# Kernel tuning notes

Measured on AMD Instinct MI355X. Metric: run time of the kernel, lower is better.

The kernel has to match this reference:

```python
import jax, jax.numpy as jnp
import numpy as np

N_NODES = 100000
N_EDGES = 3200000  # avg degree 32
NFEAT = 512
NOUT = 7
DIMS = [NFEAT, 12, 10, 8, 6, 4, NOUT]  # hard-coded hidden widths from __init__


def setup_inputs() -> dict:
    key = jax.random.key(0)
    ks = jax.random.split(key, 4 + 2 * 6)
    inp = {
        "x": jax.random.normal(ks[0], (N_NODES, NFEAT), dtype=jnp.float32),
        "edge_val": jax.random.uniform(ks[1], (N_EDGES,), dtype=jnp.float32) / 32.0,  # ~normalized adj
        "edge_src": jax.random.randint(ks[2], (N_EDGES,), 0, N_NODES),
        "edge_dst": jax.random.randint(ks[3], (N_EDGES,), 0, N_NODES),
    }
    for i in range(6):
        s = 1.0 / np.sqrt(DIMS[i + 1])  # pygcn reset_parameters: U(-1/sqrt(out), 1/sqrt(out))
        inp[f"W{i+1}"] = jax.random.uniform(ks[4 + 2 * i], (DIMS[i], DIMS[i + 1]), jnp.float32, -s, s)
        inp[f"b{i+1}"] = jax.random.uniform(ks[5 + 2 * i], (DIMS[i + 1],), jnp.float32, -s, s)
    return inp


def reference(x, edge_val, W1, b1, W2, b2, W3, b3, W4, b4, W5, b5, W6, b6,
              edge_src, edge_dst):
    n = x.shape[0]

    def gc(h, W, b):
        s = h @ W                                   # [N, out] dense mm
        m = edge_val[:, None] * s[edge_src]         # gather + scale per edge
        agg = jax.ops.segment_sum(m, edge_dst, num_segments=n)  # spmm scatter
        return agg + b

    tanhshrink = lambda v: v - jnp.tanh(v)

    h = gc(x, W1, b1)                # dropout p=0 -> identity
    h = jax.nn.relu(gc(h, W2, b2))   # eval-mode dropout -> identity
    h = tanhshrink(gc(h, W3, b3))
    h = tanhshrink(gc(h, W4, b4))
    h = gc(h, W5, b5)
    return gc(h, W6, b6)
```

## Files before the change

### kernel.cpp

```cpp
#include <hip/hip_runtime.h>
#include <math.h>
#include <stdint.h>


#define T_EDGES 12800
#define NB_MAX  1600
#define FCAP    2560
#define OTSTR   72
#define KIT     10
#define MAXIT   336

__global__ __launch_bounds__(512) void hist_kernel(const int* __restrict__ dst,
                                                   int* __restrict__ ghist, int E, int NB) {
    __shared__ int h[NB_MAX];
    for (int i = threadIdx.x; i < NB; i += 512) h[i] = 0;
    __syncthreads();
    int base = blockIdx.x * T_EDGES;
    int n = min(T_EDGES, E - base);
    for (int i = threadIdx.x; i < n; i += 512)
        atomicAdd(&h[((unsigned)dst[base + i]) >> 6], 1);
    __syncthreads();
    for (int i = threadIdx.x; i < NB; i += 512)
        ghist[(size_t)blockIdx.x * NB + i] = h[i];
}

__global__ __launch_bounds__(256) void scanC_kernel(const int* __restrict__ ghist,
                                                    int* __restrict__ goff,
                                                    int* __restrict__ btot, int NT, int NB) {
    __shared__ int part[256];
    int b = blockIdx.x, t = threadIdx.x;
    int v = (t < NT) ? ghist[(size_t)t * NB + b] : 0;
    part[t] = v;
    __syncthreads();
    for (int off = 1; off < 256; off <<= 1) {
        int x = (t >= off) ? part[t - off] : 0;
        __syncthreads();
        part[t] += x;
        __syncthreads();
    }
    if (t < NT) goff[(size_t)t * NB + b] = b * FCAP + part[t] - v;
    if (t == 255) btot[b] = part[255];
}

__global__ __launch_bounds__(1024) void scatter_kernel(const int* __restrict__ src,
                                                       const int* __restrict__ dst,
                                                       const float* __restrict__ val,
                                                       const int* __restrict__ ghist,
                                                       const int* __restrict__ goff,
                                                       int2* __restrict__ edges, int E, int NB) {
    __shared__ unsigned perm[T_EDGES];
    __shared__ int loff[NB_MAX];
    __shared__ int lcur[NB_MAX];
    __shared__ int part[1024];
    int tb = blockIdx.x, t = threadIdx.x;
    int base = tb * T_EDGES;
    int n = min(T_EDGES, E - base);

    int chunk = (NB + 1023) / 1024;
    int lo = t * chunk, hi = min(lo + chunk, NB);
    int s = 0;
    for (int i = lo; i < hi; i++) {
        int c = ghist[(size_t)tb * NB + i];
        loff[i] = c;
        s += c;
    }
    part[t] = s;
    __syncthreads();
    for (int off = 1; off < 1024; off <<= 1) {
        int x = (t >= off) ? part[t - off] : 0;
        __syncthreads();
        part[t] += x;
        __syncthreads();
    }
    int run = part[t] - s;
    for (int i = lo; i < hi; i++) {
        int c = loff[i];
        loff[i] = run;
        lcur[i] = run;
        run += c;
    }
    __syncthreads();

    for (int i = t; i < n; i += 1024) {
        int d = dst[base + i];
        unsigned b = ((unsigned)d) >> 6;
        int p = atomicAdd(&lcur[b], 1);
        perm[p] = (unsigned)i | (b << 14) | ((unsigned)(d & 63) << 25);
    }
    __syncthreads();

    for (int o = t; o < n; o += 1024) {
        unsigned v = perm[o];
        int li = v & 16383;
        int b  = (v >> 14) & 2047;
        int ld = v >> 25;
        int g  = goff[(size_t)tb * NB + b] + (o - loff[b]);
        edges[g] = make_int2(src[base + li] | (ld << 17), __float_as_int(val[base + li]));
    }
}

__global__ __launch_bounds__(512) void finalize_kernel(int2* __restrict__ edges,
                                                       const int* __restrict__ btot,
                                                       int* __restrict__ offsTab) {
    __shared__ int2 recs[FCAP];
    __shared__ int2 recs2[FCAP];
    __shared__ int cnt[64], offs[64], cur[64];
    int b = blockIdx.x, t = threadIdx.x;
    size_t s0 = (size_t)b * FCAP;
    int ne = min(btot[b], FCAP);
    if (t < 64) cnt[t] = 0;
    __syncthreads();
    for (int i = t; i < ne; i += 512) {
        int2 r = edges[s0 + i];
        recs[i] = r;
        atomicAdd(&cnt[(r.x >> 17) & 63], 1);
    }
    __syncthreads();
    if (t == 0) {
        int run = 0;
        for (int i = 0; i < 64; i++) { offs[i] = run; run += cnt[i]; }
    }
    __syncthreads();
    if (t < 64) cur[t] = offs[t];
    __syncthreads();
    for (int i = t; i < ne; i += 512) {
        int2 r = recs[i];
        int ld = (r.x >> 17) & 63;
        int p = atomicAdd(&cur[ld], 1);
        recs2[p] = r;
    }
    __syncthreads();
    for (int i = t; i < ne; i += 512) edges[s0 + i] = recs2[i];
    if (t < 64) offsTab[(size_t)b * OTSTR + t] = offs[t];
    if (t == 64) offsTab[(size_t)b * OTSTR + 64] = ne;
}

__global__ __launch_bounds__(256) void dense1_kernel(const float* __restrict__ x,
                                                     const float* __restrict__ W,
                                                     float* __restrict__ out, int N) {
    __shared__ float xs[256 * 33];
    const int t    = threadIdx.x;
    const int row0 = blockIdx.x * 256;
    const int r    = row0 + t;

    float acc[12];
#pragma unroll
    for (int j = 0; j < 12; j++) acc[j] = 0.f;

    for (int tile = 0; tile < 16; ++tile) {
#pragma unroll
        for (int i = 0; i < 8; i++) {
            int idx4 = t + 256 * i;
            int flat = idx4 * 4;
            int rl   = flat >> 5;
            int c    = flat & 31;
            int rg   = row0 + rl;
            if (rg >= N) rg = N - 1;
            const float4 v = *(const float4*)(x + (size_t)rg * 512 + tile * 32 + c);
            float* p = &xs[rl * 33 + c];
            p[0] = v.x; p[1] = v.y; p[2] = v.z; p[3] = v.w;
        }
        __syncthreads();
#pragma unroll 8
        for (int kk = 0; kk < 32; ++kk) {
            float xv = xs[t * 33 + kk];
            int k = tile * 32 + kk;
#pragma unroll
            for (int j = 0; j < 12; j++) acc[j] += xv * W[k * 12 + j];
        }
        __syncthreads();
    }
    if (r < N) {
        float4* orow = (float4*)(out + (size_t)r * 16);
        orow[0] = make_float4(acc[0], acc[1], acc[2], acc[3]);
        orow[1] = make_float4(acc[4], acc[5], acc[6], acc[7]);
        orow[2] = make_float4(acc[8], acc[9], acc[10], acc[11]);
        orow[3] = make_float4(0.f, 0.f, 0.f, 0.f);
    }
}

template <int SV, int ANV, int DIN, int DOUT, int OSTR, int ACT, bool FINAL>
__global__ __launch_bounds__(256) void layer_kernel(const int2* __restrict__ edges,
                                                    const int* __restrict__ offsTab,
                                                    const float* __restrict__ s,
                                                    const float* __restrict__ bias,
                                                    const float* __restrict__ W,
                                                    float* __restrict__ out, int N) {
    constexpr int ASTR = 13;
    __shared__ int2  ebuf[FCAP];
    __shared__ float acc[64 * ASTR];
    __shared__ int   offs[65];
    __shared__ int   items[MAXIT];
    __shared__ int   nitems_s;
    const int b = blockIdx.x, t = threadIdx.x;
    const int ne = offsTab[(size_t)b * OTSTR + 64];

    for (int i = t; i < 64 * ASTR; i += 256) acc[i] = 0.f;
    for (int i = t; i < ne; i += 256) ebuf[i] = edges[(size_t)b * FCAP + i];
    if (t < 65) offs[t] = offsTab[(size_t)b * OTSTR + t];
    if (t == 0) nitems_s = 0;
    __syncthreads();

    if (t < 64) {
        int st = offs[t];
        int c  = ((t == 63) ? ne : offs[t + 1]) - st;
        if (c > 0) {
            int ni  = (c + KIT - 1) / KIT;
            int pos = atomicAdd(&nitems_s, ni);
            for (int j = 0; j < ni; j++) {
                int len = min(KIT, c - j * KIT);
                items[pos + j] = ((st + j * KIT) << 10) | (len << 6) | t;
            }
        }
    }
    __syncthreads();

    const int nit = nitems_s;
    const float4* sv = (const float4*)s;
    for (int j = t; j < nit; j += 256) {
        int it = items[j];
        int ld    = it & 63;
        int lenm1 = ((it >> 6) & 15) - 1;
        int st    = it >> 10;
        float4 a[ANV];
#pragma unroll
        for (int v = 0; v < ANV; v++) a[v] = make_float4(0.f, 0.f, 0.f, 0.f);
#pragma unroll
        for (int k = 0; k < KIT; k++) {
            int idx = st + min(k, lenm1);
            int2 ev = ebuf[idx];
            float w = (k <= lenm1) ? __int_as_float(ev.y) : 0.f;
            const float4* srow = sv + (size_t)(ev.x & 0x1FFFF) * SV;
#pragma unroll
            for (int v = 0; v < ANV; v++) {
                float4 xr = srow[v];
                a[v].x += w * xr.x; a[v].y += w * xr.y;
                a[v].z += w * xr.z; a[v].w += w * xr.w;
            }
        }
#pragma unroll
        for (int v = 0; v < ANV; v++) {
            atomicAdd(&acc[ld * ASTR + 4 * v + 0], a[v].x);
            atomicAdd(&acc[ld * ASTR + 4 * v + 1], a[v].y);
            atomicAdd(&acc[ld * ASTR + 4 * v + 2], a[v].z);
            atomicAdd(&acc[ld * ASTR + 4 * v + 3], a[v].w);
        }
    }
    __syncthreads();

    if (t < 64) {
        int node = (b << 6) + t;
        if (node < N) {
            float h[DIN];
#pragma unroll
            for (int k = 0; k < DIN; k++) {
                float z = acc[t * ASTR + k] + bias[k];
                if (ACT == 1) z = fmaxf(z, 0.f);
                else if (ACT == 2) z = z - tanhf(z);
                h[k] = z;
            }
            if (FINAL) {
#pragma unroll
                for (int k = 0; k < DIN; k++) out[(size_t)node * DIN + k] = h[k];
            } else {
                float o[OSTR];
#pragma unroll
                for (int j = 0; j < OSTR; j++) o[j] = 0.f;
#pragma unroll
                for (int j = 0; j < DOUT; j++) {
                    float tj = 0.f;
#pragma unroll
                    for (int k = 0; k < DIN; k++) tj += h[k] * W[k * DOUT + j];
                    o[j] = tj;
                }
                float4* orow = (float4*)(out + (size_t)node * OSTR);
#pragma unroll
                for (int v = 0; v < OSTR / 4; v++)
                    orow[v] = make_float4(o[4 * v], o[4 * v + 1], o[4 * v + 2], o[4 * v + 3]);
            }
        }
    }
}


static inline size_t align256(size_t x) { return (x + 255) & ~(size_t)255; }

extern "C" void kernel_launch(void* const* d_in, const int* in_sizes, int n_in,
                              void* d_out, int out_size, void* d_ws, size_t ws_size,
                              hipStream_t stream) {
    const float* x        = (const float*)d_in[0];
    const float* edge_val = (const float*)d_in[1];
    const int*   edge_src = (const int*)d_in[2];
    const int*   edge_dst = (const int*)d_in[3];
    const float* W1 = (const float*)d_in[4];   const float* b1 = (const float*)d_in[5];
    const float* W2 = (const float*)d_in[6];   const float* b2 = (const float*)d_in[7];
    const float* W3 = (const float*)d_in[8];   const float* b3 = (const float*)d_in[9];
    const float* W4 = (const float*)d_in[10];  const float* b4 = (const float*)d_in[11];
    const float* W5 = (const float*)d_in[12];  const float* b5 = (const float*)d_in[13];
    const float* W6 = (const float*)d_in[14];  const float* b6 = (const float*)d_in[15];

    const int N = in_sizes[0] / 512;
    const int E = in_sizes[1];
    float* out = (float*)d_out;

    const int NB = (N + 63) >> 6;
    const int NT = (E + T_EDGES - 1) / T_EDGES;
    const int nb = (N + 255) / 256;

    char* w = (char*)d_ws;
    float* A       = (float*)w;  w += align256((size_t)N * 16 * sizeof(float));
    float* B       = (float*)w;  w += align256((size_t)N * 16 * sizeof(float));
    int*   ghist   = (int*)w;    w += align256((size_t)NT * NB * sizeof(int));
    int*   goff    = (int*)w;    w += align256((size_t)NT * NB * sizeof(int));
    int*   btot    = (int*)w;    w += align256((size_t)NB * sizeof(int));
    int*   offsTab = (int*)w;    w += align256((size_t)NB * OTSTR * sizeof(int));
    int2*  edges   = (int2*)w;   w += align256((size_t)NB * FCAP * sizeof(int2));

    hist_kernel<<<NT, 512, 0, stream>>>(edge_dst, ghist, E, NB);
    scanC_kernel<<<NB, 256, 0, stream>>>(ghist, goff, btot, NT, NB);
    scatter_kernel<<<NT, 1024, 0, stream>>>(edge_src, edge_dst, edge_val, ghist, goff, edges, E, NB);
    finalize_kernel<<<NB, 512, 0, stream>>>(edges, btot, offsTab);

    dense1_kernel<<<nb, 256, 0, stream>>>(x, W1, A, N);

    layer_kernel<4, 3, 12, 10, 16, 0, false><<<NB, 256, 0, stream>>>(edges, offsTab, A, b1, W2, B, N);
    layer_kernel<4, 3, 10, 8, 8, 1, false><<<NB, 256, 0, stream>>>(edges, offsTab, B, b2, W3, A, N);
    layer_kernel<2, 2, 8, 6, 8, 2, false><<<NB, 256, 0, stream>>>(edges, offsTab, A, b3, W4, B, N);
    layer_kernel<2, 2, 6, 4, 4, 2, false><<<NB, 256, 0, stream>>>(edges, offsTab, B, b4, W5, A, N);
    layer_kernel<1, 1, 4, 7, 8, 0, false><<<NB, 256, 0, stream>>>(edges, offsTab, A, b5, W6, B, N);
    layer_kernel<2, 2, 7, 7, 8, 0, true><<<NB, 256, 0, stream>>>(edges, offsTab, B, b6, (const float*)nullptr, out, N);
}
```

Before: 728.2 us.

## Drop per-node edge sort; accumulate each edge directly with LDS atomics

Removes the finalize kernel that sorted each 64-node bucket's edges by local destination and built an offset table. The layer kernels now stream edges straight from global memory two at a time (int4 loads) and do one shared-memory atomicAdd per edge per feature, instead of building per-destination work items and summing up to ten edges in registers before each atomic. This removes a kernel launch, a global read/write pass over the edges, and the staging of edges in LDS. In exchange it issues about ten times more LDS atomics per layer, with possible contention when edges in a wave share a destination.

```diff
diff --git a/kernel.cpp b/kernel.cpp
--- a/kernel.cpp
+++ b/kernel.cpp
@@ -6,9 +6,6 @@
 #define T_EDGES 12800
 #define NB_MAX  1600
 #define FCAP    2560
-#define OTSTR   72
-#define KIT     10
-#define MAXIT   336
 
 __global__ __launch_bounds__(512) void hist_kernel(const int* __restrict__ dst,
                                                    int* __restrict__ ghist, int E, int NB) {
@@ -99,42 +96,6 @@
     }
 }
 
-__global__ __launch_bounds__(512) void finalize_kernel(int2* __restrict__ edges,
-                                                       const int* __restrict__ btot,
-                                                       int* __restrict__ offsTab) {
-    __shared__ int2 recs[FCAP];
-    __shared__ int2 recs2[FCAP];
-    __shared__ int cnt[64], offs[64], cur[64];
-    int b = blockIdx.x, t = threadIdx.x;
-    size_t s0 = (size_t)b * FCAP;
-    int ne = min(btot[b], FCAP);
-    if (t < 64) cnt[t] = 0;
-    __syncthreads();
-    for (int i = t; i < ne; i += 512) {
-        int2 r = edges[s0 + i];
-        recs[i] = r;
-        atomicAdd(&cnt[(r.x >> 17) & 63], 1);
-    }
-    __syncthreads();
-    if (t == 0) {
-        int run = 0;
-        for (int i = 0; i < 64; i++) { offs[i] = run; run += cnt[i]; }
-    }
-    __syncthreads();
-    if (t < 64) cur[t] = offs[t];
-    __syncthreads();
-    for (int i = t; i < ne; i += 512) {
-        int2 r = recs[i];
-        int ld = (r.x >> 17) & 63;
-        int p = atomicAdd(&cur[ld], 1);
-        recs2[p] = r;
-    }
-    __syncthreads();
-    for (int i = t; i < ne; i += 512) edges[s0 + i] = recs2[i];
-    if (t < 64) offsTab[(size_t)b * OTSTR + t] = offs[t];
-    if (t == 64) offsTab[(size_t)b * OTSTR + 64] = ne;
-}
-
 __global__ __launch_bounds__(256) void dense1_kernel(const float* __restrict__ x,
                                                      const float* __restrict__ W,
                                                      float* __restrict__ out, int N) {
@@ -179,71 +140,56 @@
     }
 }
 
-template <int SV, int ANV, int DIN, int DOUT, int OSTR, int ACT, bool FINAL>
+template <int SV, int NACC, int DIN, int DOUT, int OSTR, int ACT, bool FINAL>
 __global__ __launch_bounds__(256) void layer_kernel(const int2* __restrict__ edges,
-                                                    const int* __restrict__ offsTab,
+                                                    const int* __restrict__ btot,
                                                     const float* __restrict__ s,
                                                     const float* __restrict__ bias,
                                                     const float* __restrict__ W,
                                                     float* __restrict__ out, int N) {
     constexpr int ASTR = 13;
-    __shared__ int2  ebuf[FCAP];
     __shared__ float acc[64 * ASTR];
-    __shared__ int   offs[65];
-    __shared__ int   items[MAXIT];
-    __shared__ int   nitems_s;
     const int b = blockIdx.x, t = threadIdx.x;
-    const int ne = offsTab[(size_t)b * OTSTR + 64];
+    const int ne = min(btot[b], FCAP);
 
     for (int i = t; i < 64 * ASTR; i += 256) acc[i] = 0.f;
-    for (int i = t; i < ne; i += 256) ebuf[i] = edges[(size_t)b * FCAP + i];
-    if (t < 65) offs[t] = offsTab[(size_t)b * OTSTR + t];
-    if (t == 0) nitems_s = 0;
-    __syncthreads();
-
-    if (t < 64) {
-        int st = offs[t];
-        int c  = ((t == 63) ? ne : offs[t + 1]) - st;
-        if (c > 0) {
-            int ni  = (c + KIT - 1) / KIT;
-            int pos = atomicAdd(&nitems_s, ni);
-            for (int j = 0; j < ni; j++) {
-                int len = min(KIT, c - j * KIT);
-                items[pos + j] = ((st + j * KIT) << 10) | (len << 6) | t;
-            }
-        }
-    }
-    __syncthreads();
-
-    const int nit = nitems_s;
+    __syncthreads();
+
     const float4* sv = (const float4*)s;
-    for (int j = t; j < nit; j += 256) {
-        int it = items[j];
-        int ld    = it & 63;
-        int lenm1 = ((it >> 6) & 15) - 1;
-        int st    = it >> 10;
-        float4 a[ANV];
-#pragma unroll
-        for (int v = 0; v < ANV; v++) a[v] = make_float4(0.f, 0.f, 0.f, 0.f);
-#pragma unroll
-        for (int k = 0; k < KIT; k++) {
-            int idx = st + min(k, lenm1);
-            int2 ev = ebuf[idx];
-            float w = (k <= lenm1) ? __int_as_float(ev.y) : 0.f;
-            const float4* srow = sv + (size_t)(ev.x & 0x1FFFF) * SV;
-#pragma unroll
-            for (int v = 0; v < ANV; v++) {
+    const int4*   ep = (const int4*)(edges + (size_t)b * FCAP);
+    const int nh = (ne + 1) >> 1;
+#pragma unroll 2
+    for (int i = t; i < nh; i += 256) {
+        int4 e2 = ep[i];
+
+        {
+            int   sidx = e2.x & 0x1FFFF;
+            int   ld   = (e2.x >> 17) & 63;
+            float w    = __int_as_float(e2.y);
+            const float4* srow = sv + (size_t)sidx * SV;
+#pragma unroll
+            for (int v = 0; v < NACC; v++) {
                 float4 xr = srow[v];
-                a[v].x += w * xr.x; a[v].y += w * xr.y;
-                a[v].z += w * xr.z; a[v].w += w * xr.w;
-            }
-        }
-#pragma unroll
-        for (int v = 0; v < ANV; v++) {
-            atomicAdd(&acc[ld * ASTR + 4 * v + 0], a[v].x);
-            atomicAdd(&acc[ld * ASTR + 4 * v + 1], a[v].y);
-            atomicAdd(&acc[ld * ASTR + 4 * v + 2], a[v].z);
-            atomicAdd(&acc[ld * ASTR + 4 * v + 3], a[v].w);
+                atomicAdd(&acc[ld * ASTR + 4 * v + 0], w * xr.x);
+                atomicAdd(&acc[ld * ASTR + 4 * v + 1], w * xr.y);
+                atomicAdd(&acc[ld * ASTR + 4 * v + 2], w * xr.z);
+                atomicAdd(&acc[ld * ASTR + 4 * v + 3], w * xr.w);
+            }
+        }
+        {
+            bool  val  = (2 * i + 1) < ne;
+            int   sidx = val ? (e2.z & 0x1FFFF) : 0;
+            int   ld   = (e2.z >> 17) & 63;
+            float w    = val ? __int_as_float(e2.w) : 0.f;
+            const float4* srow = sv + (size_t)sidx * SV;
+#pragma unroll
+            for (int v = 0; v < NACC; v++) {
+                float4 xr = srow[v];
+                atomicAdd(&acc[ld * ASTR + 4 * v + 0], w * xr.x);
+                atomicAdd(&acc[ld * ASTR + 4 * v + 1], w * xr.y);
+                atomicAdd(&acc[ld * ASTR + 4 * v + 2], w * xr.z);
+                atomicAdd(&acc[ld * ASTR + 4 * v + 3], w * xr.w);
+            }
         }
     }
     __syncthreads();
@@ -308,25 +254,23 @@
     const int nb = (N + 255) / 256;
 
     char* w = (char*)d_ws;
-    float* A       = (float*)w;  w += align256((size_t)N * 16 * sizeof(float));
-    float* B       = (float*)w;  w += align256((size_t)N * 16 * sizeof(float));
-    int*   ghist   = (int*)w;    w += align256((size_t)NT * NB * sizeof(int));
-    int*   goff    = (int*)w;    w += align256((size_t)NT * NB * sizeof(int));
-    int*   btot    = (int*)w;    w += align256((size_t)NB * sizeof(int));
-    int*   offsTab = (int*)w;    w += align256((size_t)NB * OTSTR * sizeof(int));
-    int2*  edges   = (int2*)w;   w += align256((size_t)NB * FCAP * sizeof(int2));
+    float* A     = (float*)w;  w += align256((size_t)N * 16 * sizeof(float));
+    float* B     = (float*)w;  w += align256((size_t)N * 16 * sizeof(float));
+    int*   ghist = (int*)w;    w += align256((size_t)NT * NB * sizeof(int));
+    int*   goff  = (int*)w;    w += align256((size_t)NT * NB * sizeof(int));
+    int*   btot  = (int*)w;    w += align256((size_t)NB * sizeof(int));
+    int2*  edges = (int2*)w;   w += align256((size_t)NB * FCAP * sizeof(int2));
 
     hist_kernel<<<NT, 512, 0, stream>>>(edge_dst, ghist, E, NB);
     scanC_kernel<<<NB, 256, 0, stream>>>(ghist, goff, btot, NT, NB);
     scatter_kernel<<<NT, 1024, 0, stream>>>(edge_src, edge_dst, edge_val, ghist, goff, edges, E, NB);
-    finalize_kernel<<<NB, 512, 0, stream>>>(edges, btot, offsTab);
 
     dense1_kernel<<<nb, 256, 0, stream>>>(x, W1, A, N);
 
-    layer_kernel<4, 3, 12, 10, 16, 0, false><<<NB, 256, 0, stream>>>(edges, offsTab, A, b1, W2, B, N);
-    layer_kernel<4, 3, 10, 8, 8, 1, false><<<NB, 256, 0, stream>>>(edges, offsTab, B, b2, W3, A, N);
-    layer_kernel<2, 2, 8, 6, 8, 2, false><<<NB, 256, 0, stream>>>(edges, offsTab, A, b3, W4, B, N);
-    layer_kernel<2, 2, 6, 4, 4, 2, false><<<NB, 256, 0, stream>>>(edges, offsTab, B, b4, W5, A, N);
-    layer_kernel<1, 1, 4, 7, 8, 0, false><<<NB, 256, 0, stream>>>(edges, offsTab, A, b5, W6, B, N);
-    layer_kernel<2, 2, 7, 7, 8, 0, true><<<NB, 256, 0, stream>>>(edges, offsTab, B, b6, (const float*)nullptr, out, N);
-}
+    layer_kernel<4, 3, 12, 10, 16, 0, false><<<NB, 256, 0, stream>>>(edges, btot, A, b1, W2, B, N);
+    layer_kernel<4, 3, 10, 8, 8, 1, false><<<NB, 256, 0, stream>>>(edges, btot, B, b2, W3, A, N);
+    layer_kernel<2, 2, 8, 6, 8, 2, false><<<NB, 256, 0, stream>>>(edges, btot, A, b3, W4, B, N);
+    layer_kernel<2, 2, 6, 4, 4, 2, false><<<NB, 256, 0, stream>>>(edges, btot, B, b4, W5, A, N);
+    layer_kernel<1, 1, 4, 7, 8, 0, false><<<NB, 256, 0, stream>>>(edges, btot, A, b5, W6, B, N);
+    layer_kernel<2, 2, 7, 7, 8, 0, true><<<NB, 256, 0, stream>>>(edges, btot, B, b6, (const float*)nullptr, out, N);
+}
```

New measurement: 1.411 ms. 93.7% more time.
